# Kernel optimization log

Hardware: AMD Instinct MI355X
Metric: run time of the kernel (lower is better)

## Reference

```python
import jax, jax.numpy as jnp
from jax import lax
import numpy as np

B, N, C = 8, 50000, 8
SCORE_THR = 0.99
NMS_THR = 0.5
MAX_DET = 100
K_PRE = 1024          # per-class candidate budget (>> expected ~500 survivors of the 0.99 threshold)
NEG = jnp.float32(-1e30)


def setup_inputs() -> dict:
    key = jax.random.key(0)
    k1, k2, k3, k4, k5 = jax.random.split(key, 5)
    # valid (x1,y1,x2,y2) boxes in a 512px frame
    cxy = jax.random.uniform(k1, (B, N, 2), dtype=jnp.float32) * 512.0
    wh = jax.random.uniform(k2, (B, N, 2), dtype=jnp.float32) * 96.0 + 4.0
    boxes = jnp.concatenate([cxy - wh * 0.5, cxy + wh * 0.5], axis=-1)
    classification = jax.random.uniform(k3, (B, N, C), dtype=jnp.float32)
    rotation = jax.random.normal(k4, (B, N, 3), dtype=jnp.float32)
    translation = jax.random.normal(k5, (B, N, 3), dtype=jnp.float32)
    return {"boxes": boxes, "classification": classification,
            "rotation": rotation, "translation": translation}


def _pairwise_iou(b):  # b: [K,4] -> [K,K]
    x1, y1, x2, y2 = b[:, 0], b[:, 1], b[:, 2], b[:, 3]
    area = (x2 - x1) * (y2 - y1)
    iw = jnp.maximum(jnp.minimum(x2[:, None], x2[None, :]) - jnp.maximum(x1[:, None], x1[None, :]), 0.0)
    ih = jnp.maximum(jnp.minimum(y2[:, None], y2[None, :]) - jnp.maximum(y1[:, None], y1[None, :]), 0.0)
    inter = iw * ih
    return inter / (area[:, None] + area[None, :] - inter)


def _nms_one_class(boxes_n, scores_n):
    """boxes_n [N,4], scores_n [N] -> (top_s [K], top_i [K], keep [K] bool)."""
    masked = jnp.where(scores_n > SCORE_THR, scores_n, NEG)
    top_s, top_i = lax.top_k(masked, K_PRE)       # sorted descending, like torchvision NMS ordering
    cand = boxes_n[top_i]                          # [K,4]
    valid = top_s > SCORE_THR
    iou = _pairwise_iou(cand)                      # [K,K]

    def step(keep, i):
        # suppressed if any already-kept higher-score box overlaps > NMS_THR
        suppressed = jnp.any(keep & (iou[:, i] > NMS_THR))
        keep = keep.at[i].set(valid[i] & ~suppressed)
        return keep, None

    keep, _ = lax.scan(step, jnp.zeros(K_PRE, dtype=bool), jnp.arange(K_PRE))
    return top_s, top_i, keep


def _filter(boxes, classification, rotation, translation):
    b, n, c = classification.shape
    per_class = jax.vmap(_nms_one_class, in_axes=(None, 1))      # over classes
    top_s, top_i, keep = jax.vmap(per_class)(boxes, classification)  # [B,C,K] each

    sc = jnp.where(keep, top_s, NEG).reshape(b, c * K_PRE)
    labels = jnp.broadcast_to(jnp.arange(c)[None, :, None], (b, c, K_PRE)).reshape(b, c * K_PRE)
    idx = top_i.reshape(b, c * K_PRE)

    best_s, sel = lax.top_k(sc, MAX_DET)                          # [B,100]
    sel_idx = jnp.take_along_axis(idx, sel, axis=1)
    sel_lab = jnp.take_along_axis(labels, sel, axis=1)
    ok = best_s > SCORE_THR                                       # kept scores are all > threshold

    gather = lambda x: jnp.take_along_axis(x, sel_idx[:, :, None], axis=1)
    out_boxes = jnp.where(ok[:, :, None], gather(boxes), -1.0)
    out_scores = jnp.where(ok, best_s, -1.0)
    out_labels = jnp.where(ok, sel_lab, -1).astype(jnp.int64)
    out_rot = jnp.where(ok[:, :, None], gather(rotation), -1.0)
    out_trans = jnp.where(ok[:, :, None], gather(translation), -1.0)
    return out_boxes, out_scores, out_labels, out_rot, out_trans


@jax.jit
def reference(boxes, classification, rotation, translation):
    return _filter(boxes, classification, rotation, translation)
```

## Files before the change

kernel.cpp:

```cpp
#include <hip/hip_runtime.h>
#include <stdint.h>

#define BB 8
#define NN 50000
#define SCORE_THR 0.99f
#define NMS_THR 0.5f
#define MAX_DET 100
#define K_PRE 1024
#define CAP 2048
#define KEEP_CAP 128
#define CNT_STRIDE 64
#define T_MAX 16
#define NPAIR 136
#define TRI_WORDS 8704

typedef unsigned long long u64;
typedef unsigned int u32;
typedef __attribute__((ext_vector_type(2))) unsigned long long u64x2;


__global__ void k_init(int* __restrict__ cnts) {
    for (int i = threadIdx.x; i < 64 * CNT_STRIDE + 64; i += 256) cnts[i] = 0;
}

__global__ __launch_bounds__(256) void k_filter(const float* __restrict__ cls,
                                                int* __restrict__ cand_cnt,
                                                u64* __restrict__ cand_keys) {
    __shared__ int wcnt[8][4];
    __shared__ int woff[8][4];
    __shared__ int cbase[8];
    int b = blockIdx.y;
    int tid = threadIdx.x;
    int lane = tid & 63, w = tid >> 6;
    int n = blockIdx.x * 256 + tid;
    bool vn = n < NN;
    float s[8];
    if (vn) {
        const float4* p = (const float4*)(cls + ((size_t)b * NN + n) * 8);
        float4 a = p[0], b2 = p[1];
        s[0] = a.x; s[1] = a.y; s[2] = a.z; s[3] = a.w;
        s[4] = b2.x; s[5] = b2.y; s[6] = b2.z; s[7] = b2.w;
    } else {
        #pragma unroll
        for (int c = 0; c < 8; ++c) s[c] = 0.f;
    }
    u64 bal[8];
    #pragma unroll
    for (int c = 0; c < 8; ++c) {
        bool pred = vn && (s[c] > SCORE_THR);
        bal[c] = __ballot(pred);
        if (lane == 0) wcnt[c][w] = (int)__popcll(bal[c]);
    }
    __syncthreads();
    if (tid < 8) {
        int c = tid, acc = 0;
        #pragma unroll
        for (int ww = 0; ww < 4; ++ww) { woff[c][ww] = acc; acc += wcnt[c][ww]; }
        cbase[c] = acc ? atomicAdd(&cand_cnt[(b * 8 + c) * CNT_STRIDE], acc) : 0;
    }
    __syncthreads();
    #pragma unroll
    for (int c = 0; c < 8; ++c) {
        if (vn && (s[c] > SCORE_THR)) {
            int slot = cbase[c] + woff[c][w] + (int)__popcll(bal[c] & ((1ull << lane) - 1ull));
            if (slot < CAP)
                cand_keys[(size_t)(b * 8 + c) * CAP + slot] =
                    ((u64)__float_as_uint(s[c]) << 32) | (u32)(~(u32)n);
        }
    }
}

__global__ __launch_bounds__(1024) void k_sort(const float* __restrict__ boxes,
                                               const int* __restrict__ cand_cnt,
                                               const u64* __restrict__ cand_keys,
                                               u64* __restrict__ sk_g,
                                               float4* __restrict__ box4) {
    __shared__ __align__(16) u64 sk_in[CAP];
    int tid = threadIdx.x;
    int bc = blockIdx.x;
    int b = bc >> 3;
    int cnt = cand_cnt[bc * CNT_STRIDE];
    if (cnt > CAP) cnt = CAP;
    int cnt2 = (cnt + 1) & ~1;
    for (int i = tid; i < cnt2; i += 1024)
        sk_in[i] = (i < cnt) ? cand_keys[(size_t)bc * CAP + i] : 0ull;
    __syncthreads();
    int nv = cnt2 >> 1;
    const u64x2* skv = (const u64x2*)sk_in;
    for (int g = 0; g < cnt; g += 1024) {
        int i0 = g + tid;
        u64 k0 = (i0 < cnt) ? sk_in[i0] : 0ull;
        int r0 = 0;
        #pragma unroll 4
        for (int jv = 0; jv < nv; ++jv) {
            u64x2 kk = skv[jv];
            r0 += (kk.x > k0); r0 += (kk.y > k0);
        }
        if (i0 < cnt && r0 < K_PRE) {
            sk_g[(size_t)bc * K_PRE + r0] = k0;
            u32 n = ~(u32)k0;
            box4[(size_t)bc * K_PRE + r0] =
                *(const float4*)(boxes + ((size_t)b * NN + n) * 4);
        }
    }
}

__global__ __launch_bounds__(256) void k_iou(const int* __restrict__ cand_cnt,
                                             const float4* __restrict__ box4,
                                             u64* __restrict__ rowmask) {
    int bc = blockIdx.y;
    int p = blockIdx.x;
    int cnt = cand_cnt[bc * CNT_STRIDE];
    int n_cand = cnt < K_PRE ? cnt : K_PRE;
    int ntiles = (n_cand + 63) >> 6;
    int ti = 0, acc = 0;
    while (acc + ti + 1 <= p) { acc += ti + 1; ++ti; }
    int tj = p - acc;
    if (ti >= ntiles) return;
    const float4* bx = box4 + (size_t)bc * K_PRE;
    __shared__ float4 srb[64];
    int tid = threadIdx.x;
    int lane = tid & 63, w = tid >> 6;
    if (tid < 64) srb[tid] = bx[ti * 64 + tid];
    __syncthreads();
    int cg = tj * 64 + lane;
    float4 cb = bx[cg];
    float ca = (cb.z - cb.x) * (cb.w - cb.y);
    u64* out = rowmask + (size_t)bc * TRI_WORDS + 64 * (ti * (ti + 1) / 2) + tj;
    #pragma unroll
    for (int r16 = 0; r16 < 16; ++r16) {
        int r = (w << 4) | r16;
        float4 rb = srb[r];
        float ra = (rb.z - rb.x) * (rb.w - rb.y);
        float iw = fminf(rb.z, cb.z) - fmaxf(rb.x, cb.x);
        float ih = fminf(rb.w, cb.w) - fmaxf(rb.y, cb.y);
        iw = fmaxf(iw, 0.f); ih = fmaxf(ih, 0.f);
        float inter = iw * ih;
        float iou = inter / (ra + ca - inter);
        int rg = ti * 64 + r;
        bool pr = (rg < n_cand) && (cg < n_cand) && ((ti != tj) || (lane < r)) &&
                  (iou > NMS_THR);
        u64 m = __ballot(pr);
        if (lane == 0) out[(size_t)r * (ti + 1)] = m;
    }
}

__global__ __launch_bounds__(64) void k_greedy(const int* __restrict__ cand_cnt,
                                               const u64* __restrict__ sk_g,
                                               const u64* __restrict__ rowmask,
                                               int* __restrict__ kept_cnt,
                                               u64* __restrict__ kept_keys) {
    int lane = threadIdx.x;
    int bc = blockIdx.x;
    int c = bc & 7;
    int cnt = cand_cnt[bc * CNT_STRIDE];
    int n_cand = cnt < K_PRE ? cnt : K_PRE;
    int ntiles = (n_cand + 63) >> 6;
    const u64* tri = rowmask + (size_t)bc * TRI_WORDS;
    u64 kept_w[T_MAX];
    #pragma unroll
    for (int t = 0; t < T_MAX; ++t) kept_w[t] = 0ull;
    for (int t = 0; t < ntiles; ++t) {
        int g = t * 64 + lane;
        const u64* base = tri + 64 * (t * (t + 1) / 2) + (size_t)lane * (t + 1);
        u64 supbits = 0;
        #pragma unroll
        for (int w = 0; w < T_MAX - 1; ++w)
            if (w < t) supbits |= base[w] & kept_w[w];
        u64 rowm = base[t];
        bool el = (g < n_cand) && (supbits == 0ull);
        u64 alive = __ballot(el);
        u64 kb = 0;
        while (alive) {
            int j = __ffsll(alive) - 1;
            kb |= (1ull << j);
            u64 colj = __ballot(((rowm >> j) & 1ull) != 0);
            alive &= ~(colj | (1ull << j));
        }
        #pragma unroll
        for (int w = 0; w < T_MAX; ++w)
            if (w == t) kept_w[w] = kb;
    }
    u64 lmask = (1ull << lane) - 1ull;
    int pre = 0;
    #pragma unroll
    for (int t = 0; t < T_MAX; ++t) {
        if (t < ntiles) {
            u64 kb = kept_w[t];
            if ((kb >> lane) & 1ull) {
                int rank = pre + (int)__popcll(kb & lmask);
                if (rank < KEEP_CAP) {
                    int i = t * 64 + lane;
                    u64 key = sk_g[(size_t)bc * K_PRE + i];
                    u32 sb = (u32)(key >> 32);
                    u32 n = (~(u32)key) & 0x1FFFFu;
                    int pos = c * K_PRE + i;
                    kept_keys[(size_t)bc * KEEP_CAP + rank] =
                        ((u64)sb << 30) | ((u64)(8191 - pos) << 17) | (u64)n;
                }
            }
            pre += (int)__popcll(kb);
        }
    }
    if (lane == 0) kept_cnt[bc] = pre < KEEP_CAP ? pre : KEEP_CAP;
}

__global__ __launch_bounds__(1024) void k_final(const float* __restrict__ boxes,
                                                const float* __restrict__ rot,
                                                const float* __restrict__ trans,
                                                const int* __restrict__ kept_cnt,
                                                const u64* __restrict__ kept_keys,
                                                float* __restrict__ out) {
    __shared__ u64 fk[1024];
    __shared__ int scnt[8];
    int tid = threadIdx.x;
    int b = blockIdx.x;
    int c = tid >> 7, i = tid & 127;
    if (tid < 8) scnt[tid] = kept_cnt[b * 8 + tid];
    int cc = kept_cnt[b * 8 + c];
    u64 key = (i < cc) ? kept_keys[(size_t)(b * 8 + c) * KEEP_CAP + i] : 0ull;
    fk[tid] = key;
    __syncthreads();
    int total = 0;
    #pragma unroll
    for (int r = 0; r < 8; ++r) total += scnt[r];
    if (i < cc) {
        int rank = i;
        #pragma unroll
        for (int r = 0; r < 8; ++r) {
            if (r == c) continue;
            int basei = r << 7;
            int lo;
            if (fk[basei + 127] > key) lo = 128;
            else {
                lo = 0;
                #pragma unroll
                for (int s = 64; s > 0; s >>= 1)
                    if (fk[basei + lo + s - 1] > key) lo += s;
            }
            rank += lo;
        }
        if (rank < MAX_DET) {
            u32 n = (u32)(key & 0x1FFFFu);
            int pos = 8191 - (int)((key >> 17) & 0x1FFFu);
            int cls = pos >> 10;
            float osc = __uint_as_float((u32)(key >> 30));
            const float* bp = boxes + ((size_t)b * NN + n) * 4;
            const float* rp = rot + ((size_t)b * NN + n) * 3;
            const float* tp = trans + ((size_t)b * NN + n) * 3;
            int base = b * MAX_DET + rank;
            out[base * 4 + 0] = bp[0];
            out[base * 4 + 1] = bp[1];
            out[base * 4 + 2] = bp[2];
            out[base * 4 + 3] = bp[3];
            out[BB * MAX_DET * 4 + base] = osc;
            out[BB * MAX_DET * 5 + base] = (float)cls;
            float* ro = out + BB * MAX_DET * 6;
            ro[base * 3 + 0] = rp[0];
            ro[base * 3 + 1] = rp[1];
            ro[base * 3 + 2] = rp[2];
            float* to = out + BB * MAX_DET * 6 + BB * MAX_DET * 3;
            to[base * 3 + 0] = tp[0];
            to[base * 3 + 1] = tp[1];
            to[base * 3 + 2] = tp[2];
        }
    }
    if (tid < MAX_DET && tid >= total) {
        int base = b * MAX_DET + tid;
        out[base * 4 + 0] = -1.f;
        out[base * 4 + 1] = -1.f;
        out[base * 4 + 2] = -1.f;
        out[base * 4 + 3] = -1.f;
        out[BB * MAX_DET * 4 + base] = -1.f;
        out[BB * MAX_DET * 5 + base] = -1.f;
        float* ro = out + BB * MAX_DET * 6;
        ro[base * 3 + 0] = -1.f;
        ro[base * 3 + 1] = -1.f;
        ro[base * 3 + 2] = -1.f;
        float* to = out + BB * MAX_DET * 6 + BB * MAX_DET * 3;
        to[base * 3 + 0] = -1.f;
        to[base * 3 + 1] = -1.f;
        to[base * 3 + 2] = -1.f;
    }
}

extern "C" void kernel_launch(void* const* d_in, const int* in_sizes, int n_in,
                              void* d_out, int out_size, void* d_ws, size_t ws_size,
                              hipStream_t stream) {
    const float* boxes = (const float*)d_in[0];
    const float* cls   = (const float*)d_in[1];
    const float* rot   = (const float*)d_in[2];
    const float* trans = (const float*)d_in[3];
    char* ws = (char*)d_ws;
    int* cand_cnt  = (int*)ws;
    int* kept_cnt  = (int*)(ws + 16384);
    u64* cand_keys = (u64*)(ws + 16896);
    u64* kept_keys = (u64*)(ws + 1065472);
    u64* sk_g      = (u64*)(ws + 1131008);
    float4* box4   = (float4*)(ws + 1655296);
    u64* rowmask   = (u64*)(ws + 2703872);
    float* out = (float*)d_out;

    hipLaunchKernelGGL(k_init, dim3(1), dim3(256), 0, stream, cand_cnt);
    hipLaunchKernelGGL(k_filter, dim3((NN + 255) / 256, BB), dim3(256), 0, stream,
                       cls, cand_cnt, cand_keys);
    hipLaunchKernelGGL(k_sort, dim3(64), dim3(1024), 0, stream,
                       boxes, cand_cnt, cand_keys, sk_g, box4);
    hipLaunchKernelGGL(k_iou, dim3(NPAIR, 64), dim3(256), 0, stream,
                       cand_cnt, box4, rowmask);
    hipLaunchKernelGGL(k_greedy, dim3(64), dim3(64), 0, stream,
                       cand_cnt, sk_g, rowmask, kept_cnt, kept_keys);
    hipLaunchKernelGGL(k_final, dim3(BB), dim3(1024), 0, stream,
                       boxes, rot, trans, kept_cnt, kept_keys, out);
}
```

Baseline: 139.0 us.

## Fuse greedy NMS into final merge kernel and split rank-sort across many blocks

The per-class greedy suppression and the final cross-class top-100 merge become one kernel. Each batch block runs the eight class greedies in its first eight wavefronts and writes kept keys straight into shared memory, which removes one launch and the global kept-key round trip. The rank sort now runs as many 64-thread blocks, each ranking 64 keys against the full candidate list, instead of one 1024-thread block per class, for more parallelism across CUs. In exchange, every small block reloads the whole candidate list into LDS, and the greedy stage now uses only 8 blocks of the GPU.

```diff
diff --git a/kernel.cpp b/kernel.cpp
--- a/kernel.cpp
+++ b/kernel.cpp
@@ -20,7 +20,7 @@
 
 
 __global__ void k_init(int* __restrict__ cnts) {
-    for (int i = threadIdx.x; i < 64 * CNT_STRIDE + 64; i += 256) cnts[i] = 0;
+    for (int i = threadIdx.x; i < 64 * CNT_STRIDE; i += 256) cnts[i] = 0;
 }
 
 __global__ __launch_bounds__(256) void k_filter(const float* __restrict__ cls,
@@ -70,38 +70,38 @@
     }
 }
 
-__global__ __launch_bounds__(1024) void k_sort(const float* __restrict__ boxes,
-                                               const int* __restrict__ cand_cnt,
-                                               const u64* __restrict__ cand_keys,
-                                               u64* __restrict__ sk_g,
-                                               float4* __restrict__ box4) {
+__global__ __launch_bounds__(64) void k_sort(const float* __restrict__ boxes,
+                                             const int* __restrict__ cand_cnt,
+                                             const u64* __restrict__ cand_keys,
+                                             u64* __restrict__ sk_g,
+                                             float4* __restrict__ box4) {
     __shared__ __align__(16) u64 sk_in[CAP];
-    int tid = threadIdx.x;
-    int bc = blockIdx.x;
+    int lane = threadIdx.x;
+    int q = blockIdx.x;
+    int bc = blockIdx.y;
     int b = bc >> 3;
     int cnt = cand_cnt[bc * CNT_STRIDE];
     if (cnt > CAP) cnt = CAP;
+    if (q * 64 >= cnt) return;
     int cnt2 = (cnt + 1) & ~1;
-    for (int i = tid; i < cnt2; i += 1024)
+    for (int i = lane; i < cnt2; i += 64)
         sk_in[i] = (i < cnt) ? cand_keys[(size_t)bc * CAP + i] : 0ull;
     __syncthreads();
+    int i0 = q * 64 + lane;
+    u64 k0 = (i0 < cnt) ? sk_in[i0] : 0ull;
+    int r0 = 0;
     int nv = cnt2 >> 1;
     const u64x2* skv = (const u64x2*)sk_in;
-    for (int g = 0; g < cnt; g += 1024) {
-        int i0 = g + tid;
-        u64 k0 = (i0 < cnt) ? sk_in[i0] : 0ull;
-        int r0 = 0;
-        #pragma unroll 4
-        for (int jv = 0; jv < nv; ++jv) {
-            u64x2 kk = skv[jv];
-            r0 += (kk.x > k0); r0 += (kk.y > k0);
-        }
-        if (i0 < cnt && r0 < K_PRE) {
-            sk_g[(size_t)bc * K_PRE + r0] = k0;
-            u32 n = ~(u32)k0;
-            box4[(size_t)bc * K_PRE + r0] =
-                *(const float4*)(boxes + ((size_t)b * NN + n) * 4);
-        }
+    #pragma unroll 4
+    for (int jv = 0; jv < nv; ++jv) {
+        u64x2 kk = skv[jv];
+        r0 += (kk.x > k0); r0 += (kk.y > k0);
+    }
+    if (i0 < cnt && r0 < K_PRE) {
+        sk_g[(size_t)bc * K_PRE + r0] = k0;
+        u32 n = ~(u32)k0;
+        box4[(size_t)bc * K_PRE + r0] =
+            *(const float4*)(boxes + ((size_t)b * NN + n) * 4);
     }
 }
 
@@ -145,82 +145,78 @@
     }
 }
 
-__global__ __launch_bounds__(64) void k_greedy(const int* __restrict__ cand_cnt,
+__global__ __launch_bounds__(1024) void k_fuse(const float* __restrict__ boxes,
+                                               const float* __restrict__ rot,
+                                               const float* __restrict__ trans,
+                                               const int* __restrict__ cand_cnt,
                                                const u64* __restrict__ sk_g,
                                                const u64* __restrict__ rowmask,
-                                               int* __restrict__ kept_cnt,
-                                               u64* __restrict__ kept_keys) {
-    int lane = threadIdx.x;
-    int bc = blockIdx.x;
-    int c = bc & 7;
-    int cnt = cand_cnt[bc * CNT_STRIDE];
-    int n_cand = cnt < K_PRE ? cnt : K_PRE;
-    int ntiles = (n_cand + 63) >> 6;
-    const u64* tri = rowmask + (size_t)bc * TRI_WORDS;
-    u64 kept_w[T_MAX];
-    #pragma unroll
-    for (int t = 0; t < T_MAX; ++t) kept_w[t] = 0ull;
-    for (int t = 0; t < ntiles; ++t) {
-        int g = t * 64 + lane;
-        const u64* base = tri + 64 * (t * (t + 1) / 2) + (size_t)lane * (t + 1);
-        u64 supbits = 0;
-        #pragma unroll
-        for (int w = 0; w < T_MAX - 1; ++w)
-            if (w < t) supbits |= base[w] & kept_w[w];
-        u64 rowm = base[t];
-        bool el = (g < n_cand) && (supbits == 0ull);
-        u64 alive = __ballot(el);
-        u64 kb = 0;
-        while (alive) {
-            int j = __ffsll(alive) - 1;
-            kb |= (1ull << j);
-            u64 colj = __ballot(((rowm >> j) & 1ull) != 0);
-            alive &= ~(colj | (1ull << j));
-        }
-        #pragma unroll
-        for (int w = 0; w < T_MAX; ++w)
-            if (w == t) kept_w[w] = kb;
-    }
-    u64 lmask = (1ull << lane) - 1ull;
-    int pre = 0;
-    #pragma unroll
-    for (int t = 0; t < T_MAX; ++t) {
-        if (t < ntiles) {
-            u64 kb = kept_w[t];
-            if ((kb >> lane) & 1ull) {
-                int rank = pre + (int)__popcll(kb & lmask);
-                if (rank < KEEP_CAP) {
-                    int i = t * 64 + lane;
-                    u64 key = sk_g[(size_t)bc * K_PRE + i];
-                    u32 sb = (u32)(key >> 32);
-                    u32 n = (~(u32)key) & 0x1FFFFu;
-                    int pos = c * K_PRE + i;
-                    kept_keys[(size_t)bc * KEEP_CAP + rank] =
-                        ((u64)sb << 30) | ((u64)(8191 - pos) << 17) | (u64)n;
-                }
-            }
-            pre += (int)__popcll(kb);
-        }
-    }
-    if (lane == 0) kept_cnt[bc] = pre < KEEP_CAP ? pre : KEEP_CAP;
-}
-
-__global__ __launch_bounds__(1024) void k_final(const float* __restrict__ boxes,
-                                                const float* __restrict__ rot,
-                                                const float* __restrict__ trans,
-                                                const int* __restrict__ kept_cnt,
-                                                const u64* __restrict__ kept_keys,
-                                                float* __restrict__ out) {
+                                               float* __restrict__ out) {
     __shared__ u64 fk[1024];
     __shared__ int scnt[8];
     int tid = threadIdx.x;
+    int lane = tid & 63, w = tid >> 6;
     int b = blockIdx.x;
+    fk[tid] = 0ull;
+    __syncthreads();
+    if (w < 8) {
+        int c = w;
+        int bc = b * 8 + c;
+        int cnt = cand_cnt[bc * CNT_STRIDE];
+        int n_cand = cnt < K_PRE ? cnt : K_PRE;
+        int ntiles = (n_cand + 63) >> 6;
+        const u64* tri = rowmask + (size_t)bc * TRI_WORDS;
+        u64 kept_w[T_MAX];
+        #pragma unroll
+        for (int t = 0; t < T_MAX; ++t) kept_w[t] = 0ull;
+        for (int t = 0; t < ntiles; ++t) {
+            int g = t * 64 + lane;
+            const u64* base = tri + 64 * (t * (t + 1) / 2) + (size_t)lane * (t + 1);
+            u64 supbits = 0;
+            #pragma unroll
+            for (int ww = 0; ww < T_MAX - 1; ++ww)
+                if (ww < t) supbits |= base[ww] & kept_w[ww];
+            u64 rowm = base[t];
+            bool el = (g < n_cand) && (supbits == 0ull);
+            u64 alive = __ballot(el);
+            u64 kb = 0;
+            while (alive) {
+                int j = __ffsll(alive) - 1;
+                kb |= (1ull << j);
+                u64 colj = __ballot(((rowm >> j) & 1ull) != 0);
+                alive &= ~(colj | (1ull << j));
+            }
+            #pragma unroll
+            for (int ww = 0; ww < T_MAX; ++ww)
+                if (ww == t) kept_w[ww] = kb;
+        }
+        u64 lmask = (1ull << lane) - 1ull;
+        int pre = 0;
+        #pragma unroll
+        for (int t = 0; t < T_MAX; ++t) {
+            if (t < ntiles) {
+                u64 kb = kept_w[t];
+                if ((kb >> lane) & 1ull) {
+                    int rank = pre + (int)__popcll(kb & lmask);
+                    if (rank < KEEP_CAP) {
+                        int i = t * 64 + lane;
+                        u64 key = sk_g[(size_t)bc * K_PRE + i];
+                        u32 sb = (u32)(key >> 32);
+                        u32 n = (~(u32)key) & 0x1FFFFu;
+                        int pos = c * K_PRE + i;
+                        fk[c * KEEP_CAP + rank] =
+                            ((u64)sb << 30) | ((u64)(8191 - pos) << 17) | (u64)n;
+                    }
+                }
+                pre += (int)__popcll(kb);
+            }
+        }
+        if (lane == 0) scnt[c] = pre < KEEP_CAP ? pre : KEEP_CAP;
+    }
+    __syncthreads();
     int c = tid >> 7, i = tid & 127;
-    if (tid < 8) scnt[tid] = kept_cnt[b * 8 + tid];
-    int cc = kept_cnt[b * 8 + c];
-    u64 key = (i < cc) ? kept_keys[(size_t)(b * 8 + c) * KEEP_CAP + i] : 0ull;
-    fk[tid] = key;
-    __syncthreads();
+    int cc = scnt[c];
+    u64 key = fk[tid];
     int total = 0;
     #pragma unroll
     for (int r = 0; r < 8; ++r) total += scnt[r];
@@ -293,23 +289,19 @@
     const float* trans = (const float*)d_in[3];
     char* ws = (char*)d_ws;
     int* cand_cnt  = (int*)ws;
-    int* kept_cnt  = (int*)(ws + 16384);
     u64* cand_keys = (u64*)(ws + 16896);
-    u64* kept_keys = (u64*)(ws + 1065472);
-    u64* sk_g      = (u64*)(ws + 1131008);
-    float4* box4   = (float4*)(ws + 1655296);
-    u64* rowmask   = (u64*)(ws + 2703872);
+    u64* sk_g      = (u64*)(ws + 1065472);
+    float4* box4   = (float4*)(ws + 1589760);
+    u64* rowmask   = (u64*)(ws + 2638336);
     float* out = (float*)d_out;
 
     hipLaunchKernelGGL(k_init, dim3(1), dim3(256), 0, stream, cand_cnt);
     hipLaunchKernelGGL(k_filter, dim3((NN + 255) / 256, BB), dim3(256), 0, stream,
                        cls, cand_cnt, cand_keys);
-    hipLaunchKernelGGL(k_sort, dim3(64), dim3(1024), 0, stream,
+    hipLaunchKernelGGL(k_sort, dim3(CAP / 64, 64), dim3(64), 0, stream,
                        boxes, cand_cnt, cand_keys, sk_g, box4);
     hipLaunchKernelGGL(k_iou, dim3(NPAIR, 64), dim3(256), 0, stream,
                        cand_cnt, box4, rowmask);
-    hipLaunchKernelGGL(k_greedy, dim3(64), dim3(64), 0, stream,
-                       cand_cnt, sk_g, rowmask, kept_cnt, kept_keys);
-    hipLaunchKernelGGL(k_final, dim3(BB), dim3(1024), 0, stream,
-                       boxes, rot, trans, kept_cnt, kept_keys, out);
-}
+    hipLaunchKernelGGL(k_fuse, dim3(BB), dim3(1024), 0, stream,
+                       boxes, rot, trans, cand_cnt, sk_g, rowmask, out);
+}
```

New measurement: 144.2 us. +3.7%, slower.

## Fuse sort, IoU and greedy NMS into one block kernel; drop atomic compaction

Applied to the files above, without the earlier changes.

Fuses the per-class sort, pairwise IoU mask and greedy suppression into one 1024-thread kernel per (batch, class). Boxes, areas and sorted keys stay in LDS instead of making global round trips. The filter kernel now writes fixed per-block slots plus counts, compacted later with a wave prefix scan, which removes the init kernel and the global atomics. This cuts launches from six to three. The cost is IoU work done by only 64 blocks instead of a wide grid, and candidates beyond 32 per 256-element block are silently dropped.

```diff
diff --git a/kernel.cpp b/kernel.cpp
--- a/kernel.cpp
+++ b/kernel.cpp
@@ -9,9 +9,9 @@
 #define K_PRE 1024
 #define CAP 2048
 #define KEEP_CAP 128
-#define CNT_STRIDE 64
+#define NBLK 196
+#define SLOT_MAX 32
 #define T_MAX 16
-#define NPAIR 136
 #define TRI_WORDS 8704
 
 typedef unsigned long long u64;
@@ -19,20 +19,16 @@
 typedef __attribute__((ext_vector_type(2))) unsigned long long u64x2;
 
 
-__global__ void k_init(int* __restrict__ cnts) {
-    for (int i = threadIdx.x; i < 64 * CNT_STRIDE + 64; i += 256) cnts[i] = 0;
-}
-
 __global__ __launch_bounds__(256) void k_filter(const float* __restrict__ cls,
-                                                int* __restrict__ cand_cnt,
-                                                u64* __restrict__ cand_keys) {
+                                                int* __restrict__ blkcnt,
+                                                u64* __restrict__ cand_blk) {
     __shared__ int wcnt[8][4];
     __shared__ int woff[8][4];
-    __shared__ int cbase[8];
+    int gx = blockIdx.x;
     int b = blockIdx.y;
     int tid = threadIdx.x;
     int lane = tid & 63, w = tid >> 6;
-    int n = blockIdx.x * 256 + tid;
+    int n = gx * 256 + tid;
     bool vn = n < NN;
     float s[8];
     if (vn) {
@@ -56,40 +52,80 @@
         int c = tid, acc = 0;
         #pragma unroll
         for (int ww = 0; ww < 4; ++ww) { woff[c][ww] = acc; acc += wcnt[c][ww]; }
-        cbase[c] = acc ? atomicAdd(&cand_cnt[(b * 8 + c) * CNT_STRIDE], acc) : 0;
+        blkcnt[(b * 8 + c) * NBLK + gx] = acc < SLOT_MAX ? acc : SLOT_MAX;
     }
     __syncthreads();
     #pragma unroll
     for (int c = 0; c < 8; ++c) {
         if (vn && (s[c] > SCORE_THR)) {
-            int slot = cbase[c] + woff[c][w] + (int)__popcll(bal[c] & ((1ull << lane) - 1ull));
-            if (slot < CAP)
-                cand_keys[(size_t)(b * 8 + c) * CAP + slot] =
+            int slot = woff[c][w] + (int)__popcll(bal[c] & ((1ull << lane) - 1ull));
+            if (slot < SLOT_MAX)
+                cand_blk[((size_t)(b * 8 + c) * NBLK + gx) * SLOT_MAX + slot] =
                     ((u64)__float_as_uint(s[c]) << 32) | (u32)(~(u32)n);
         }
     }
 }
 
-__global__ __launch_bounds__(1024) void k_sort(const float* __restrict__ boxes,
-                                               const int* __restrict__ cand_cnt,
-                                               const u64* __restrict__ cand_keys,
-                                               u64* __restrict__ sk_g,
-                                               float4* __restrict__ box4) {
-    __shared__ __align__(16) u64 sk_in[CAP];
+__global__ __launch_bounds__(1024) void k_nmsall(const float* __restrict__ boxes,
+                                                 const int* __restrict__ blkcnt,
+                                                 const u64* __restrict__ cand_blk,
+                                                 u64* __restrict__ rowmask,
+                                                 int* __restrict__ kept_cnt,
+                                                 u64* __restrict__ kept_keys) {
+    __shared__ __align__(16) u64 skin[CAP];
+    __shared__ u64 sk[K_PRE];
+    __shared__ float4 box4L[K_PRE];
+    __shared__ float areaL[K_PRE];
+    __shared__ int scntb[NBLK];
+    __shared__ int pref[NBLK];
+    __shared__ int cntTotS;
     int tid = threadIdx.x;
+    int lane = tid & 63, w = tid >> 6;
     int bc = blockIdx.x;
+    int c = bc & 7;
     int b = bc >> 3;
-    int cnt = cand_cnt[bc * CNT_STRIDE];
+    if (tid < NBLK) scntb[tid] = blkcnt[bc * NBLK + tid];
+    __syncthreads();
+    if (w == 0) {
+        int carry = 0;
+        #pragma unroll
+        for (int r = 0; r < 4; ++r) {
+            int idx = r * 64 + lane;
+            int v = (idx < NBLK) ? scntb[idx] : 0;
+            int x = v;
+            #pragma unroll
+            for (int d = 1; d < 64; d <<= 1) {
+                int t = __shfl_up(x, d);
+                if (lane >= d) x += t;
+            }
+            if (idx < NBLK) pref[idx] = carry + x - v;
+            carry += __shfl(x, 63);
+        }
+        if (lane == 0) cntTotS = carry;
+    }
+    __syncthreads();
+    int cnt = cntTotS;
     if (cnt > CAP) cnt = CAP;
+    if (tid < NBLK * 4) {
+        int blk = tid >> 2, part = tid & 3;
+        int cb = scntb[blk];
+        int base = pref[blk];
+        int k0 = part * 8, k1 = k0 + 8; if (k1 > cb) k1 = cb;
+        const u64* src = cand_blk + ((size_t)bc * NBLK + blk) * SLOT_MAX;
+        for (int k = k0; k < k1; ++k) {
+            int dst = base + k;
+            if (dst < CAP) skin[dst] = src[k];
+        }
+    }
+    __syncthreads();
+    if (tid == 0 && (cnt & 1)) skin[cnt] = 0ull;
+    __syncthreads();
     int cnt2 = (cnt + 1) & ~1;
-    for (int i = tid; i < cnt2; i += 1024)
-        sk_in[i] = (i < cnt) ? cand_keys[(size_t)bc * CAP + i] : 0ull;
-    __syncthreads();
     int nv = cnt2 >> 1;
-    const u64x2* skv = (const u64x2*)sk_in;
+    const u64x2* skv = (const u64x2*)skin;
     for (int g = 0; g < cnt; g += 1024) {
         int i0 = g + tid;
-        u64 k0 = (i0 < cnt) ? sk_in[i0] : 0ull;
+        u64 k0 = (i0 < cnt) ? skin[i0] : 0ull;
         int r0 = 0;
         #pragma unroll 4
         for (int jv = 0; jv < nv; ++jv) {
@@ -97,112 +133,97 @@
             r0 += (kk.x > k0); r0 += (kk.y > k0);
         }
         if (i0 < cnt && r0 < K_PRE) {
-            sk_g[(size_t)bc * K_PRE + r0] = k0;
+            sk[r0] = k0;
             u32 n = ~(u32)k0;
-            box4[(size_t)bc * K_PRE + r0] =
-                *(const float4*)(boxes + ((size_t)b * NN + n) * 4);
-        }
-    }
-}
-
-__global__ __launch_bounds__(256) void k_iou(const int* __restrict__ cand_cnt,
-                                             const float4* __restrict__ box4,
-                                             u64* __restrict__ rowmask) {
-    int bc = blockIdx.y;
-    int p = blockIdx.x;
-    int cnt = cand_cnt[bc * CNT_STRIDE];
+            float4 b4 = *(const float4*)(boxes + ((size_t)b * NN + n) * 4);
+            box4L[r0] = b4;
+            areaL[r0] = (b4.z - b4.x) * (b4.w - b4.y);
+        }
+    }
+    __syncthreads();
     int n_cand = cnt < K_PRE ? cnt : K_PRE;
     int ntiles = (n_cand + 63) >> 6;
-    int ti = 0, acc = 0;
-    while (acc + ti + 1 <= p) { acc += ti + 1; ++ti; }
-    int tj = p - acc;
-    if (ti >= ntiles) return;
-    const float4* bx = box4 + (size_t)bc * K_PRE;
-    __shared__ float4 srb[64];
-    int tid = threadIdx.x;
-    int lane = tid & 63, w = tid >> 6;
-    if (tid < 64) srb[tid] = bx[ti * 64 + tid];
-    __syncthreads();
-    int cg = tj * 64 + lane;
-    float4 cb = bx[cg];
-    float ca = (cb.z - cb.x) * (cb.w - cb.y);
-    u64* out = rowmask + (size_t)bc * TRI_WORDS + 64 * (ti * (ti + 1) / 2) + tj;
-    #pragma unroll
-    for (int r16 = 0; r16 < 16; ++r16) {
-        int r = (w << 4) | r16;
-        float4 rb = srb[r];
-        float ra = (rb.z - rb.x) * (rb.w - rb.y);
-        float iw = fminf(rb.z, cb.z) - fmaxf(rb.x, cb.x);
-        float ih = fminf(rb.w, cb.w) - fmaxf(rb.y, cb.y);
-        iw = fmaxf(iw, 0.f); ih = fmaxf(ih, 0.f);
-        float inter = iw * ih;
-        float iou = inter / (ra + ca - inter);
-        int rg = ti * 64 + r;
-        bool pr = (rg < n_cand) && (cg < n_cand) && ((ti != tj) || (lane < r)) &&
-                  (iou > NMS_THR);
-        u64 m = __ballot(pr);
-        if (lane == 0) out[(size_t)r * (ti + 1)] = m;
-    }
-}
-
-__global__ __launch_bounds__(64) void k_greedy(const int* __restrict__ cand_cnt,
-                                               const u64* __restrict__ sk_g,
-                                               const u64* __restrict__ rowmask,
-                                               int* __restrict__ kept_cnt,
-                                               u64* __restrict__ kept_keys) {
-    int lane = threadIdx.x;
-    int bc = blockIdx.x;
-    int c = bc & 7;
-    int cnt = cand_cnt[bc * CNT_STRIDE];
-    int n_cand = cnt < K_PRE ? cnt : K_PRE;
-    int ntiles = (n_cand + 63) >> 6;
-    const u64* tri = rowmask + (size_t)bc * TRI_WORDS;
-    u64 kept_w[T_MAX];
-    #pragma unroll
-    for (int t = 0; t < T_MAX; ++t) kept_w[t] = 0ull;
-    for (int t = 0; t < ntiles; ++t) {
-        int g = t * 64 + lane;
-        const u64* base = tri + 64 * (t * (t + 1) / 2) + (size_t)lane * (t + 1);
-        u64 supbits = 0;
-        #pragma unroll
-        for (int w = 0; w < T_MAX - 1; ++w)
-            if (w < t) supbits |= base[w] & kept_w[w];
-        u64 rowm = base[t];
-        bool el = (g < n_cand) && (supbits == 0ull);
-        u64 alive = __ballot(el);
-        u64 kb = 0;
-        while (alive) {
-            int j = __ffsll(alive) - 1;
-            kb |= (1ull << j);
-            u64 colj = __ballot(((rowm >> j) & 1ull) != 0);
-            alive &= ~(colj | (1ull << j));
-        }
-        #pragma unroll
-        for (int w = 0; w < T_MAX; ++w)
-            if (w == t) kept_w[w] = kb;
-    }
-    u64 lmask = (1ull << lane) - 1ull;
-    int pre = 0;
-    #pragma unroll
-    for (int t = 0; t < T_MAX; ++t) {
-        if (t < ntiles) {
-            u64 kb = kept_w[t];
-            if ((kb >> lane) & 1ull) {
-                int rank = pre + (int)__popcll(kb & lmask);
-                if (rank < KEEP_CAP) {
-                    int i = t * 64 + lane;
-                    u64 key = sk_g[(size_t)bc * K_PRE + i];
-                    u32 sb = (u32)(key >> 32);
-                    u32 n = (~(u32)key) & 0x1FFFFu;
-                    int pos = c * K_PRE + i;
-                    kept_keys[(size_t)bc * KEEP_CAP + rank] =
-                        ((u64)sb << 30) | ((u64)(8191 - pos) << 17) | (u64)n;
+    int npairs = ntiles * (ntiles + 1) / 2;
+    {
+        int tg = tid >> 8;
+        int sub = (tid >> 6) & 3;
+        u64* rm = rowmask + (size_t)bc * TRI_WORDS;
+        for (int p = tg; p < npairs; p += 4) {
+            int ti = 0, acc = 0;
+            while (acc + ti + 1 <= p) { acc += ti + 1; ++ti; }
+            int tj = p - acc;
+            int cg = tj * 64 + lane;
+            float4 cb = box4L[cg];
+            float ca = areaL[cg];
+            u64* outw = rm + 64 * (ti * (ti + 1) / 2) + tj;
+            #pragma unroll
+            for (int r16 = 0; r16 < 16; ++r16) {
+                int r = (sub << 4) | r16;
+                float4 rb = box4L[ti * 64 + r];
+                float ra = areaL[ti * 64 + r];
+                float iw = fminf(rb.z, cb.z) - fmaxf(rb.x, cb.x);
+                float ih = fminf(rb.w, cb.w) - fmaxf(rb.y, cb.y);
+                iw = fmaxf(iw, 0.f); ih = fmaxf(ih, 0.f);
+                float inter = iw * ih;
+                float iou = inter / (ra + ca - inter);
+                int rg = ti * 64 + r;
+                bool pr = (rg < n_cand) && (cg < n_cand) && ((ti != tj) || (lane < r)) &&
+                          (iou > NMS_THR);
+                u64 m = __ballot(pr);
+                if (lane == 0) outw[(size_t)r * (ti + 1)] = m;
+            }
+        }
+    }
+    __syncthreads();
+    if (w == 0) {
+        const u64* tri = rowmask + (size_t)bc * TRI_WORDS;
+        u64 kept_w[T_MAX];
+        #pragma unroll
+        for (int t = 0; t < T_MAX; ++t) kept_w[t] = 0ull;
+        for (int t = 0; t < ntiles; ++t) {
+            const u64* base = tri + 64 * (t * (t + 1) / 2) + (size_t)lane * (t + 1);
+            u64 supbits = 0;
+            #pragma unroll
+            for (int ww = 0; ww < T_MAX - 1; ++ww)
+                if (ww < t) supbits |= base[ww] & kept_w[ww];
+            u64 rowm = base[t];
+            int g = t * 64 + lane;
+            bool el = (g < n_cand) && (supbits == 0ull);
+            u64 alive = __ballot(el);
+            u64 kb = 0;
+            while (alive) {
+                int j = __ffsll(alive) - 1;
+                kb |= (1ull << j);
+                u64 colj = __ballot(((rowm >> j) & 1ull) != 0);
+                alive &= ~(colj | (1ull << j));
+            }
+            #pragma unroll
+            for (int ww = 0; ww < T_MAX; ++ww)
+                if (ww == t) kept_w[ww] = kb;
+        }
+        u64 lmask = (1ull << lane) - 1ull;
+        int pre = 0;
+        #pragma unroll
+        for (int t = 0; t < T_MAX; ++t) {
+            if (t < ntiles) {
+                u64 kb = kept_w[t];
+                if ((kb >> lane) & 1ull) {
+                    int rank = pre + (int)__popcll(kb & lmask);
+                    if (rank < KEEP_CAP) {
+                        int i = t * 64 + lane;
+                        u64 key = sk[i];
+                        u32 sb = (u32)(key >> 32);
+                        u32 n = (~(u32)key) & 0x1FFFFu;
+                        int pos = c * K_PRE + i;
+                        kept_keys[(size_t)bc * KEEP_CAP + rank] =
+                            ((u64)sb << 30) | ((u64)(8191 - pos) << 17) | (u64)n;
+                    }
                 }
-            }
-            pre += (int)__popcll(kb);
-        }
-    }
-    if (lane == 0) kept_cnt[bc] = pre < KEEP_CAP ? pre : KEEP_CAP;
+                pre += (int)__popcll(kb);
+            }
+        }
+        if (lane == 0) kept_cnt[bc] = pre < KEEP_CAP ? pre : KEEP_CAP;
+    }
 }
 
 __global__ __launch_bounds__(1024) void k_final(const float* __restrict__ boxes,
@@ -292,24 +313,17 @@
     const float* rot   = (const float*)d_in[2];
     const float* trans = (const float*)d_in[3];
     char* ws = (char*)d_ws;
-    int* cand_cnt  = (int*)ws;
-    int* kept_cnt  = (int*)(ws + 16384);
-    u64* cand_keys = (u64*)(ws + 16896);
-    u64* kept_keys = (u64*)(ws + 1065472);
-    u64* sk_g      = (u64*)(ws + 1131008);
-    float4* box4   = (float4*)(ws + 1655296);
-    u64* rowmask   = (u64*)(ws + 2703872);
+    int* blkcnt    = (int*)ws;
+    u64* cand_blk  = (u64*)(ws + 51200);
+    u64* rowmask   = (u64*)(ws + 3262464);
+    u64* kept_keys = (u64*)(ws + 7718912);
+    int* kept_cnt  = (int*)(ws + 7784448);
     float* out = (float*)d_out;
 
-    hipLaunchKernelGGL(k_init, dim3(1), dim3(256), 0, stream, cand_cnt);
-    hipLaunchKernelGGL(k_filter, dim3((NN + 255) / 256, BB), dim3(256), 0, stream,
-                       cls, cand_cnt, cand_keys);
-    hipLaunchKernelGGL(k_sort, dim3(64), dim3(1024), 0, stream,
-                       boxes, cand_cnt, cand_keys, sk_g, box4);
-    hipLaunchKernelGGL(k_iou, dim3(NPAIR, 64), dim3(256), 0, stream,
-                       cand_cnt, box4, rowmask);
-    hipLaunchKernelGGL(k_greedy, dim3(64), dim3(64), 0, stream,
-                       cand_cnt, sk_g, rowmask, kept_cnt, kept_keys);
+    hipLaunchKernelGGL(k_filter, dim3(NBLK, BB), dim3(256), 0, stream,
+                       cls, blkcnt, cand_blk);
+    hipLaunchKernelGGL(k_nmsall, dim3(64), dim3(1024), 0, stream,
+                       boxes, blkcnt, cand_blk, rowmask, kept_cnt, kept_keys);
     hipLaunchKernelGGL(k_final, dim3(BB), dim3(1024), 0, stream,
                        boxes, rot, trans, kept_cnt, kept_keys, out);
 }
```

New measurement: 172.2 us. 1.24x slower.
